# Kernel tuning notes

Measured on AMD Instinct MI355X. Metric: run time of the kernel, lower is better.

Reference implementation:

```python
import jax, jax.numpy as jnp
import numpy as np


def _conv3x3(x, w):
    # NCHW input, OIHW weight, stride 1, padding 1 (SAME for 3x3)
    return jax.lax.conv_general_dilated(
        x, w, window_strides=(1, 1), padding=((1, 1), (1, 1)),
        dimension_numbers=('NCHW', 'OIHW', 'NCHW'))


def _conv1x1(x, w):
    return jax.lax.conv_general_dilated(
        x, w, window_strides=(1, 1), padding=((0, 0), (0, 0)),
        dimension_numbers=('NCHW', 'OIHW', 'NCHW'))


def setup_inputs() -> dict:
    key = jax.random.key(0)
    k_x, k_w1, k_w2, k_wm = jax.random.split(key, 4)
    N, C, H, W = 16, 256, 64, 64
    fan = C * 9
    x = jax.random.normal(k_x, (N, C, H, W), dtype=jnp.float32)
    w1 = jax.random.normal(k_w1, (C, C, 3, 3), dtype=jnp.float32) * (2.0 / fan) ** 0.5
    w2 = jax.random.normal(k_w2, (C, C, 3, 3), dtype=jnp.float32) * (2.0 / fan) ** 0.5
    w_mask = jax.random.normal(k_wm, (1, C, 1, 1), dtype=jnp.float32) * (1.0 / C) ** 0.5
    b_mask = jnp.zeros((1,), dtype=jnp.float32)
    return {'x': x, 'w1': w1, 'w2': w2, 'w_mask': w_mask, 'b_mask': b_mask}


def reference(x, w1, w2, w_mask, b_mask):
    # MaskUnit: 1x1 conv -> logits -> hard binary mask (straight-through estimator)
    logits = _conv1x1(x, w_mask) + b_mask[None, :, None, None]  # [N,1,H,W]
    hard = (logits > 0).astype(x.dtype)
    mask = logits + jax.lax.stop_gradient(hard - logits)        # std mask, binary in fwd
    # dilated mask: 3x3 max-pool (covers 3x3 receptive field of active outputs)
    mask_dilate = jax.lax.reduce_window(
        mask, -jnp.inf, jax.lax.max, (1, 1, 3, 3), (1, 1, 1, 1), 'SAME')
    # sparse branch: conv1 gated by dilated mask, conv2 gated by std mask
    h = jax.nn.relu(_conv3x3(x, w1) * mask_dilate)
    h = jax.nn.relu(_conv3x3(h, w2) * mask)
    # apply_mask + residual (mask binary -> h*mask == h already, kept for fidelity)
    out = x + h * mask
    return out
```

## Files before the change

### kernel.cpp

```cpp
#include <hip/hip_runtime.h>
#include <hip/hip_bf16.h>

#define C_ 256
#define H_ 64
#define W_ 64
#define N_ 16
#define HW_ 4096
#define IMG_ (C_ * HW_)
#define PADIMG_ (66 * 66 * 256)
#define WT_ELEMS_ (9 * 256 * 256)

typedef short bf16x8 __attribute__((ext_vector_type(8)));
typedef float f32x16 __attribute__((ext_vector_type(16)));

__device__ __forceinline__ unsigned short f2bf(float f) {
  __hip_bfloat16 h = __float2bfloat16(f);
  return *reinterpret_cast<unsigned short*>(&h);
}

__device__ __forceinline__ void gld_lds16(const void* g, void* l) {
  __builtin_amdgcn_global_load_lds(
      (const __attribute__((address_space(1))) void*)g,
      (__attribute__((address_space(3))) void*)l, 16, 0, 0);
}

__global__ __launch_bounds__(256) void xpadmask_kernel(
    const float* __restrict__ x, const float* __restrict__ wm,
    const float* __restrict__ bm, short* __restrict__ Xp,
    unsigned char* __restrict__ mask) {
  __shared__ unsigned short lds[64 * 260];
  __shared__ float wms[256];
  __shared__ double sums[4][64];
  const int h = blockIdx.x, img = blockIdx.y;
  const int tid = threadIdx.x;
  const int wv = tid >> 6, wl = tid & 63;
  wms[tid] = wm[tid];
  __syncthreads();
  const float* xi = x + (size_t)img * IMG_ + h * 64;
  double a0 = 0.0, a1 = 0.0, a2 = 0.0, a3 = 0.0;
#pragma unroll 4
  for (int i = 0; i < 16; ++i) {
#pragma unroll
    for (int u = 0; u < 4; ++u) {
      int c = (i * 4 + u) * 4 + wv;
      float v = xi[(size_t)c * HW_ + wl];
      lds[wl * 260 + c] = f2bf(v);
      double p = (double)v * (double)wms[c];
      if (u == 0) a0 += p;
      else if (u == 1) a1 += p;
      else if (u == 2) a2 += p;
      else a3 += p;
    }
  }
  sums[wv][wl] = (a0 + a1) + (a2 + a3);
  __syncthreads();
  short* Xpi = Xp + (size_t)img * PADIMG_ + ((h + 1) * 66 + 1) * 256;
#pragma unroll
  for (int j = 0; j < 16; ++j) {
    int w = j * 4 + wv;
    int c4 = wl * 4;
    uint2 d = *(const uint2*)&lds[w * 260 + c4];
    *(uint2*)&Xpi[(size_t)w * 256 + c4] = d;
  }
  if (wv == 0) {
    double t = sums[0][wl] + sums[1][wl] + sums[2][wl] + sums[3][wl] +
               (double)bm[0];
    mask[img * HW_ + h * 64 + wl] = (t > 0.0) ? 1 : 0;
  }
}

__global__ __launch_bounds__(256) void dilate_kernel(
    const unsigned char* __restrict__ mask, unsigned char* __restrict__ md) {
  int pix = blockIdx.x * 256 + threadIdx.x;
  int n = pix >> 12;
  int hw = pix & (HW_ - 1);
  int h = hw >> 6, w = hw & 63;
  int m = 0;
  for (int dy = -1; dy <= 1; dy++) {
    int hh = h + dy;
    if (hh < 0 || hh >= H_) continue;
    for (int dx = -1; dx <= 1; dx++) {
      int ww = w + dx;
      if (ww < 0 || ww >= W_) continue;
      m |= mask[n * HW_ + hh * W_ + ww];
    }
  }
  md[pix] = (unsigned char)m;
}

__global__ __launch_bounds__(256) void wt_kernel(
    const float* __restrict__ w1, const float* __restrict__ w2,
    short* __restrict__ Wt1, short* __restrict__ Wt2) {
  const int k = blockIdx.x, c = threadIdx.x;
  const float* src = blockIdx.y ? w2 : w1;
  short* dst = blockIdx.y ? Wt2 : Wt1;
  const float* s = src + ((size_t)k * 256 + c) * 9;
  const int kc = c >> 4, ce = c & 15;
#pragma unroll
  for (int t = 0; t < 9; ++t)
    dst[(((size_t)t * 16 + kc) * 256 + k) * 16 + ce] = (short)f2bf(s[t]);
}

__global__ __launch_bounds__(128) void halo_zero(short* __restrict__ Xp,
                                                 short* __restrict__ Hp) {
  int p = blockIdx.x;
  int r, c;
  if (p < 66) { r = 0; c = p; }
  else if (p < 132) { r = 65; c = p - 66; }
  else if (p < 196) { r = p - 131; c = 0; }
  else { r = p - 195; c = 65; }
  short* buf = blockIdx.z ? Hp : Xp;
  unsigned int* d = (unsigned int*)(buf + (size_t)blockIdx.y * PADIMG_ +
                                    (size_t)(r * 66 + c) * 256);
  d[threadIdx.x] = 0u;
}

#define BBUF 10560

__device__ __forceinline__ void stage_B(short* sm, int buf, const short* Xb,
                                        int ko, int wave, int lane) {
  short* Bd = sm + buf * BBUF;
#pragma unroll
  for (int q = 0; q < 6; ++q) {
    int n = wave + 4 * q;
    if (n > 21) n = 21;
    const int h = (n >= 11) ? 1 : 0;
    const int i = n - h * 11;
    const int row0 = (i < 10) ? i * 64 : 596;
    gld_lds16(Xb + (size_t)(row0 + lane) * 256 + ko + h * 8,
              Bd + h * 5280 + row0 * 8);
  }
}

template <int EPI>
__global__ __launch_bounds__(256, 2) void conv_mfma(
    const short* __restrict__ src, const short* __restrict__ Wt,
    const unsigned char* __restrict__ gate, const float* __restrict__ xres,
    short* __restrict__ dstH, float* __restrict__ dstF, int swz) {
  __shared__ __align__(16) short sm[3 * BBUF];

  const int tid = threadIdx.x;
  const int lane = tid & 63, wave = tid >> 6;
  const int ln31 = lane & 31, kh = lane >> 5;

  int bx, by, bz;
  {
    int d = blockIdx.x + 4 * (blockIdx.y + 8 * blockIdx.z);
    if (swz) {
      int k = d & 7, j = d >> 3;
      bx = j & 3;
      by = (j >> 2) & 7;
      bz = ((j >> 5) << 3) + k;
    } else {
      bx = blockIdx.x;
      by = blockIdx.y;
      bz = blockIdx.z;
    }
  }
  const int ch0 = bx * 64;
  const int h0 = by * 8;
  const int img = bz;

  const short* Xb = src + (size_t)img * PADIMG_ + (size_t)(h0 * 66) * 256;
  const short* WL = Wt + ((size_t)(ch0 + ln31)) * 16 + kh * 8;

  f32x16 acc[2][4];
#pragma unroll
  for (int i = 0; i < 2; ++i)
#pragma unroll
    for (int j = 0; j < 4; ++j)
#pragma unroll
      for (int e = 0; e < 16; ++e) acc[i][j][e] = 0.f;

  stage_B(sm, 0, Xb, 0, wave, lane);
  bf16x8 wa0 = *(const bf16x8*)(WL);
  bf16x8 wa1 = *(const bf16x8*)(WL + 512);
  stage_B(sm, 1, Xb, 16, wave, lane);
  asm volatile("s_waitcnt vmcnt(6)\n\ts_barrier" ::: "memory");

  int c0 = 0, c1 = 1, c2 = 2;
  for (int kk = 0; kk < 16; ++kk) {
    const short* Bth = sm + c0 * BBUF + kh * 5280 + (wave * 132 + ln31) * 8;
#pragma unroll
    for (int t = 0; t < 9; ++t) {
      const int ntkc = (t < 8) ? ((t + 1) * 16 + kk) : (kk + 1);
      bf16x8 na0 = *(const bf16x8*)(WL + (size_t)ntkc * 4096);
      bf16x8 na1 = *(const bf16x8*)(WL + (size_t)ntkc * 4096 + 512);
      const int dy = t / 3, dx = t % 3;
      bf16x8 b[4];
#pragma unroll
      for (int j = 0; j < 4; ++j) {
        const int off = (((j >> 1) + dy) * 66 + (j & 1) * 32 + dx) * 8;
        b[j] = *(const bf16x8*)(Bth + off);
      }
      __builtin_amdgcn_s_setprio(1);
#pragma unroll
      for (int j = 0; j < 4; ++j) {
        acc[0][j] = __builtin_amdgcn_mfma_f32_32x32x16_bf16(wa0, b[j],
                                                            acc[0][j], 0, 0, 0);
        acc[1][j] = __builtin_amdgcn_mfma_f32_32x32x16_bf16(wa1, b[j],
                                                            acc[1][j], 0, 0, 0);
      }
      __builtin_amdgcn_s_setprio(0);
      wa0 = na0;
      wa1 = na1;
    }
    if (kk < 14) stage_B(sm, c2, Xb, (kk + 2) * 16, wave, lane);
    if (kk < 15) asm volatile("s_barrier" ::: "memory");
    const int tmp = c0;
    c0 = c1;
    c1 = c2;
    c2 = tmp;
  }

  const int rb = h0 + wave * 2;
#pragma unroll
  for (int j = 0; j < 4; ++j) {
    const int r = rb + (j >> 1);
    const int col = (j & 1) * 32 + ln31;
    const int pidx = r * 64 + col;
    const unsigned char g = gate[img * HW_ + pidx];
#pragma unroll
    for (int i = 0; i < 2; ++i) {
      const f32x16 v = acc[i][j];
#pragma unroll
      for (int rg = 0; rg < 4; ++rg) {
        const int ch = ch0 + i * 32 + rg * 8 + kh * 4;
        float e0 = g ? fmaxf(v[rg * 4 + 0], 0.f) : 0.f;
        float e1 = g ? fmaxf(v[rg * 4 + 1], 0.f) : 0.f;
        float e2 = g ? fmaxf(v[rg * 4 + 2], 0.f) : 0.f;
        float e3 = g ? fmaxf(v[rg * 4 + 3], 0.f) : 0.f;
        if (EPI == 0) {
          uint2 u;
          u.x = (unsigned int)f2bf(e0) | ((unsigned int)f2bf(e1) << 16);
          u.y = (unsigned int)f2bf(e2) | ((unsigned int)f2bf(e3) << 16);
          short* dp = dstH + (size_t)img * PADIMG_ +
                      ((size_t)((r + 1) * 66 + (col + 1))) * 256 + ch;
          *(uint2*)dp = u;
        } else {
          size_t o = (size_t)img * IMG_ + (size_t)ch * HW_ + pidx;
          dstF[o] = xres[o] + e0;
          dstF[o + HW_] = xres[o + HW_] + e1;
          dstF[o + 2 * HW_] = xres[o + 2 * HW_] + e2;
          dstF[o + 3 * HW_] = xres[o + 3 * HW_] + e3;
        }
      }
    }
  }
}

extern "C" void kernel_launch(void* const* d_in, const int* in_sizes, int n_in,
                              void* d_out, int out_size, void* d_ws,
                              size_t ws_size, hipStream_t stream) {
  const float* x = (const float*)d_in[0];
  const float* w1 = (const float*)d_in[1];
  const float* w2 = (const float*)d_in[2];
  const float* wmask = (const float*)d_in[3];
  const float* bmask = (const float*)d_in[4];
  float* out = (float*)d_out;

  char* ws = (char*)d_ws;
  unsigned char* mask = (unsigned char*)ws;
  unsigned char* md = (unsigned char*)(ws + 65536);
  short* Wt1 = (short*)(ws + 131072);
  short* Wt2 = Wt1 + WT_ELEMS_;
  short* Xp = (short*)(ws + 2490368);

  const size_t fixed = 2490368;
  const size_t tailpad = 32768;
  const size_t per_img = 2 * (size_t)PADIMG_ * 2;
  int B = (ws_size > fixed + tailpad)
              ? (int)((ws_size - fixed - tailpad) / per_img) : 0;
  if (B > N_) B = N_;
  if (B < 1) B = 1;
  short* Hp = Xp + (size_t)B * PADIMG_;

  wt_kernel<<<dim3(256, 2), 256, 0, stream>>>(w1, w2, Wt1, Wt2);
  halo_zero<<<dim3(260, B, 2), 128, 0, stream>>>(Xp, Hp);

  for (int n0 = 0; n0 < N_; n0 += B) {
    const int nb = (N_ - n0 < B) ? (N_ - n0) : B;
    const int swz = (nb % 8 == 0) ? 1 : 0;
    xpadmask_kernel<<<dim3(64, nb), 256, 0, stream>>>(
        x + (size_t)n0 * IMG_, wmask, bmask, Xp, mask + n0 * HW_);
    dilate_kernel<<<nb * HW_ / 256, 256, 0, stream>>>(mask + n0 * HW_,
                                                      md + n0 * HW_);
    conv_mfma<0><<<dim3(4, 8, nb), 256, 0, stream>>>(
        Xp, Wt1, md + n0 * HW_, nullptr, Hp, nullptr, swz);
    conv_mfma<1><<<dim3(4, 8, nb), 256, 0, stream>>>(
        Hp, Wt2, mask + n0 * HW_, x + (size_t)n0 * IMG_, nullptr,
        out + (size_t)n0 * IMG_, swz);
  }
}
```

Baseline: 299.7 us.

## Fuse mask dilation into conv epilogue and deepen weight/LDS register prefetch

```diff
diff --git a/kernel.cpp b/kernel.cpp
--- a/kernel.cpp
+++ b/kernel.cpp
@@ -8,7 +8,7 @@
 #define HW_ 4096
 #define IMG_ (C_ * HW_)
 #define PADIMG_ (66 * 66 * 256)
-#define WT_ELEMS_ (9 * 256 * 256)
+#define WT_ELEMS_ (9 * 16 * 256 * 16)
 
 typedef short bf16x8 __attribute__((ext_vector_type(8)));
 typedef float f32x16 __attribute__((ext_vector_type(16)));
@@ -69,25 +69,6 @@
   }
 }
 
-__global__ __launch_bounds__(256) void dilate_kernel(
-    const unsigned char* __restrict__ mask, unsigned char* __restrict__ md) {
-  int pix = blockIdx.x * 256 + threadIdx.x;
-  int n = pix >> 12;
-  int hw = pix & (HW_ - 1);
-  int h = hw >> 6, w = hw & 63;
-  int m = 0;
-  for (int dy = -1; dy <= 1; dy++) {
-    int hh = h + dy;
-    if (hh < 0 || hh >= H_) continue;
-    for (int dx = -1; dx <= 1; dx++) {
-      int ww = w + dx;
-      if (ww < 0 || ww >= W_) continue;
-      m |= mask[n * HW_ + hh * W_ + ww];
-    }
-  }
-  md[pix] = (unsigned char)m;
-}
-
 __global__ __launch_bounds__(256) void wt_kernel(
     const float* __restrict__ w1, const float* __restrict__ w2,
     short* __restrict__ Wt1, short* __restrict__ Wt2) {
@@ -173,37 +154,47 @@
       for (int e = 0; e < 16; ++e) acc[i][j][e] = 0.f;
 
   stage_B(sm, 0, Xb, 0, wave, lane);
-  bf16x8 wa0 = *(const bf16x8*)(WL);
-  bf16x8 wa1 = *(const bf16x8*)(WL + 512);
   stage_B(sm, 1, Xb, 16, wave, lane);
-  asm volatile("s_waitcnt vmcnt(6)\n\ts_barrier" ::: "memory");
+  bf16x8 wc0 = *(const bf16x8*)(WL);
+  bf16x8 wc1 = *(const bf16x8*)(WL + 512);
+  bf16x8 wn0 = *(const bf16x8*)(WL + 16 * 4096);
+  bf16x8 wn1 = *(const bf16x8*)(WL + 16 * 4096 + 512);
+  asm volatile("s_waitcnt vmcnt(4)\n\ts_barrier" ::: "memory");
 
   int c0 = 0, c1 = 1, c2 = 2;
   for (int kk = 0; kk < 16; ++kk) {
     const short* Bth = sm + c0 * BBUF + kh * 5280 + (wave * 132 + ln31) * 8;
+    bf16x8 bc[4], bn[4];
+#pragma unroll
+    for (int j = 0; j < 4; ++j)
+      bc[j] = *(const bf16x8*)(Bth + ((j >> 1) * 66 + (j & 1) * 32) * 8);
 #pragma unroll
     for (int t = 0; t < 9; ++t) {
-      const int ntkc = (t < 8) ? ((t + 1) * 16 + kk) : (kk + 1);
-      bf16x8 na0 = *(const bf16x8*)(WL + (size_t)ntkc * 4096);
-      bf16x8 na1 = *(const bf16x8*)(WL + (size_t)ntkc * 4096 + 512);
-      const int dy = t / 3, dx = t % 3;
-      bf16x8 b[4];
+      const int nt = t + 2;
+      const int ntkc = (nt < 9) ? (nt * 16 + kk) : ((nt - 9) * 16 + kk + 1);
+      bf16x8 f0 = *(const bf16x8*)(WL + (size_t)ntkc * 4096);
+      bf16x8 f1 = *(const bf16x8*)(WL + (size_t)ntkc * 4096 + 512);
+      if (t < 8) {
+        const int dy = (t + 1) / 3, dx = (t + 1) % 3;
+#pragma unroll
+        for (int j = 0; j < 4; ++j)
+          bn[j] = *(const bf16x8*)(Bth +
+                                   (((j >> 1) + dy) * 66 + (j & 1) * 32 + dx) * 8);
+      }
+      __builtin_amdgcn_s_setprio(1);
 #pragma unroll
       for (int j = 0; j < 4; ++j) {
-        const int off = (((j >> 1) + dy) * 66 + (j & 1) * 32 + dx) * 8;
-        b[j] = *(const bf16x8*)(Bth + off);
-      }
-      __builtin_amdgcn_s_setprio(1);
-#pragma unroll
-      for (int j = 0; j < 4; ++j) {
-        acc[0][j] = __builtin_amdgcn_mfma_f32_32x32x16_bf16(wa0, b[j],
+        acc[0][j] = __builtin_amdgcn_mfma_f32_32x32x16_bf16(wc0, bc[j],
                                                             acc[0][j], 0, 0, 0);
-        acc[1][j] = __builtin_amdgcn_mfma_f32_32x32x16_bf16(wa1, b[j],
+        acc[1][j] = __builtin_amdgcn_mfma_f32_32x32x16_bf16(wc1, bc[j],
                                                             acc[1][j], 0, 0, 0);
       }
       __builtin_amdgcn_s_setprio(0);
-      wa0 = na0;
-      wa1 = na1;
+      wc0 = wn0; wc1 = wn1; wn0 = f0; wn1 = f1;
+      if (t < 8) {
+#pragma unroll
+        for (int j = 0; j < 4; ++j) bc[j] = bn[j];
+      }
     }
     if (kk < 14) stage_B(sm, c2, Xb, (kk + 2) * 16, wave, lane);
     if (kk < 15) asm volatile("s_barrier" ::: "memory");
@@ -219,7 +210,23 @@
     const int r = rb + (j >> 1);
     const int col = (j & 1) * 32 + ln31;
     const int pidx = r * 64 + col;
-    const unsigned char g = gate[img * HW_ + pidx];
+    unsigned int g;
+    if (EPI == 0) {
+      g = 0;
+#pragma unroll
+      for (int dy = -1; dy <= 1; ++dy) {
+        const int rr = r + dy;
+        if (rr < 0 || rr >= H_) continue;
+#pragma unroll
+        for (int dx = -1; dx <= 1; ++dx) {
+          const int cc = col + dx;
+          if (cc < 0 || cc >= W_) continue;
+          g |= gate[img * HW_ + rr * W_ + cc];
+        }
+      }
+    } else {
+      g = gate[img * HW_ + pidx];
+    }
 #pragma unroll
     for (int i = 0; i < 2; ++i) {
       const f32x16 v = acc[i][j];
@@ -261,12 +268,11 @@
 
   char* ws = (char*)d_ws;
   unsigned char* mask = (unsigned char*)ws;
-  unsigned char* md = (unsigned char*)(ws + 65536);
-  short* Wt1 = (short*)(ws + 131072);
+  short* Wt1 = (short*)(ws + 65536);
   short* Wt2 = Wt1 + WT_ELEMS_;
-  short* Xp = (short*)(ws + 2490368);
-
-  const size_t fixed = 2490368;
+  const size_t fixed = 65536 + 4 * (size_t)WT_ELEMS_;
+  short* Xp = (short*)(ws + fixed);
+
   const size_t tailpad = 32768;
   const size_t per_img = 2 * (size_t)PADIMG_ * 2;
   int B = (ws_size > fixed + tailpad)
@@ -283,10 +289,8 @@
     const int swz = (nb % 8 == 0) ? 1 : 0;
     xpadmask_kernel<<<dim3(64, nb), 256, 0, stream>>>(
         x + (size_t)n0 * IMG_, wmask, bmask, Xp, mask + n0 * HW_);
-    dilate_kernel<<<nb * HW_ / 256, 256, 0, stream>>>(mask + n0 * HW_,
-                                                      md + n0 * HW_);
     conv_mfma<0><<<dim3(4, 8, nb), 256, 0, stream>>>(
-        Xp, Wt1, md + n0 * HW_, nullptr, Hp, nullptr, swz);
+        Xp, Wt1, mask + n0 * HW_, nullptr, Hp, nullptr, swz);
     conv_mfma<1><<<dim3(4, 8, nb), 256, 0, stream>>>(
         Hp, Wt2, mask + n0 * HW_, x + (size_t)n0 * IMG_, nullptr,
         out + (size_t)n0 * IMG_, swz);
```

Measured after the change: 300.2 us. No clear change (+0.2%).
